# Kernel tuning notes

Hardware: AMD Instinct MI355X
Metric: run time of the kernel (lower is better)

## Reference

```python
import jax, jax.numpy as jnp
import numpy as np

B, M, H, D = 2, 16384, 8, 64
HID = H * D
SEG = 128          # segment_lengths[0]
DIL = 2            # dilation_rates[0]


def _hilbert_perm(m):
    """perm[d] = row-major token index of the d-th point on the Hilbert curve
    over an n x n grid (n = sqrt(m), power of 2). Vectorized d2xy."""
    n = int(round(np.sqrt(m)))
    assert n * n == m and (n & (n - 1)) == 0
    t = np.arange(m, dtype=np.int64)
    x = np.zeros(m, np.int64)
    y = np.zeros(m, np.int64)
    s = 1
    while s < n:
        rx = 1 & (t // 2)
        ry = 1 & (t ^ rx)
        swap = ry == 0
        flip = swap & (rx == 1)
        xf = np.where(flip, s - 1 - x, x)
        yf = np.where(flip, s - 1 - y, y)
        x, y = np.where(swap, yf, xf), np.where(swap, xf, yf)
        x = x + s * rx
        y = y + s * ry
        t = t // 4
        s *= 2
    return y * n + x


_PERM = _hilbert_perm(M)
_INV = np.empty(M, np.int64)
_INV[_PERM] = np.arange(M)
PERM = jnp.asarray(_PERM)
INV_PERM = jnp.asarray(_INV)


def setup_inputs() -> dict:
    key = jax.random.key(0)
    ks = jax.random.split(key, 8)
    sc = 0.02
    return {
        "q": jax.random.normal(ks[0], (B, M, H, D), jnp.float32),
        "k": jax.random.normal(ks[1], (B, M, H, D), jnp.float32),
        "v": jax.random.normal(ks[2], (B, M, H, D), jnp.float32),
        # wrapper projections (nn.Linear without bias; stored [in, out])
        "Wq": jax.random.normal(ks[3], (HID, HID), jnp.float32) * sc,
        "Wk": jax.random.normal(ks[4], (HID, HID), jnp.float32) * sc,
        "Wv": jax.random.normal(ks[5], (HID, HID), jnp.float32) * sc,
        # HilbertAttentionCore fused qkv projection
        "Wqkv": jax.random.normal(ks[6], (HID, 3 * HID), jnp.float32) * sc,
        # wrapper output projection
        "Wout": jax.random.normal(ks[7], (HID, HID), jnp.float32) * sc,
    }


def _hilbert_attention(x, Wqkv):
    """x: [B, M, HID] -> [B, M, HID]. Hilbert reorder + segmented dilated attn."""
    b, m, _ = x.shape
    qkv = x @ Wqkv                                    # [B, M, 3*HID]
    qkv = qkv.reshape(b, m, 3, H, D)
    # Hilbert-curve reordering of the sequence (gather)
    qkv = qkv[:, PERM]                                # [B, M, 3, H, D]
    nseg = m // SEG
    g = SEG // DIL                                    # tokens per dilated group
    # [B, nseg, g, DIL, 3, H, D]: group r holds positions r, r+DIL, ... in seg
    qkv = qkv.reshape(b, nseg, g, DIL, 3, H, D)
    qh, kh, vh = qkv[..., 0, :, :], qkv[..., 1, :, :], qkv[..., 2, :, :]
    scale = 1.0 / jnp.sqrt(jnp.asarray(D, x.dtype))
    # attention within each (segment, dilation-group): t,s index the g tokens
    scores = jnp.einsum("bntrhd,bnsrhd->bnrhts", qh, kh) * scale
    attn = jax.nn.softmax(scores, axis=-1)
    out = jnp.einsum("bnrhts,bnsrhd->bntrhd", attn, vh)
    out = out.reshape(b, m, H, D)
    # inverse Hilbert reordering (scatter back)
    out = out[:, INV_PERM]
    return out.reshape(b, m, HID)


def reference(q, k, v, Wq, Wk, Wv, Wqkv, Wout):
    b, m, h, d = q.shape
    q_flat = q.reshape(b, m, h * d)
    k_flat = k.reshape(b, m, h * d)
    v_flat = v.reshape(b, m, h * d)
    x = (q_flat @ Wq + k_flat @ Wk + v_flat @ Wv) / 3.0
    out = _hilbert_attention(x, Wqkv)
    out = out @ Wout
    return out.reshape(b, m, h, d)
```

## Files before the change

### kernel.cpp

```cpp
#include <hip/hip_runtime.h>
#include <hip/hip_bf16.h>
#include <stdint.h>


typedef __bf16 bf16_t;
typedef __bf16 bf16x8 __attribute__((ext_vector_type(8)));
typedef float  f32x4  __attribute__((ext_vector_type(4)));

#define DEVI __device__ __forceinline__
#define BAR __builtin_amdgcn_s_barrier()

static constexpr int Mtok = 16384;
static constexpr int ROWS = 32768;

DEVI void gload_lds16(const void* g, void* l) {
  __builtin_amdgcn_global_load_lds(
      (__attribute__((address_space(1))) uint32_t*)(uintptr_t)g,
      (__attribute__((address_space(3))) uint32_t*)(uint32_t)(uintptr_t)l,
      16, 0, 0);
}

DEVI void xcd_swizzle(int gx, int* bx, int* by) {
  int nwg = gx * gridDim.y;
  int wg = blockIdx.x + gx * blockIdx.y;
  int swz = (wg & 7) * (nwg >> 3) + (wg >> 3);
  *bx = swz % gx;
  *by = swz / gx;
}

__global__ void k_perm(int* __restrict__ perm) {
  int d = blockIdx.x * 256 + threadIdx.x;
  if (d >= Mtok) return;
  int t = d, x = 0, y = 0;
  for (int s = 1; s < 128; s <<= 1) {
    int rx = (t >> 1) & 1;
    int ry = (t ^ rx) & 1;
    if (ry == 0) {
      if (rx == 1) { x = s - 1 - x; y = s - 1 - y; }
      int tmp = x; x = y; y = tmp;
    }
    x += s * rx;
    y += s * ry;
    t >>= 2;
  }
  perm[d] = y * 128 + x;
}

__global__ void k_prep_w(const float* __restrict__ Wq, const float* __restrict__ Wk,
                         const float* __restrict__ Wv, const float* __restrict__ Wqkv,
                         const float* __restrict__ Wout,
                         bf16_t* __restrict__ W1t, bf16_t* __restrict__ Wqkvt,
                         bf16_t* __restrict__ Woutt) {
  const int tid = blockIdx.x * 256 + threadIdx.x;
  const int stride = gridDim.x * 256;
  for (int i = tid; i < 512 * 1536; i += stride) {
    int n = i / 1536, kk = i % 1536;
    const float* W = (kk < 512) ? Wq : (kk < 1024 ? Wk : Wv);
    W1t[i] = (bf16_t)(W[(kk & 511) * 512 + n] * (1.0f / 3.0f));
  }
  for (int i = tid; i < 1536 * 512; i += stride) {
    int n = i / 512, kk = i % 512;
    Wqkvt[i] = (bf16_t)Wqkv[kk * 1536 + n];
  }
  for (int i = tid; i < 512 * 512; i += stride) {
    int n = i / 512, kk = i % 512;
    Woutt[i] = (bf16_t)Wout[kk * 512 + n];
  }
}

DEVI void stageB(const bf16_t* Bb, int Kdim, int k0, bf16_t* dst, int qsel,
                 int tid, int cswz) {
  int r = tid >> 3;
  int rb0 = (r >> 5) * 64 + qsel * 32 + (r & 31);
  const bf16_t* g = Bb + (long)rb0 * Kdim + k0 + cswz * 8;
  gload_lds16(g, dst + rb0 * 64 + (tid & 7) * 8);
  gload_lds16(g + (long)128 * Kdim, dst + (rb0 + 128) * 64 + (tid & 7) * 8);
}

DEVI void stageA(const bf16_t* Ab, int Kdim, int k0, bf16_t* dst, int qsel,
                 int tid, int cswz) {
  int r = tid >> 3;
  int row0 = r + qsel * 64;
  const bf16_t* g = Ab + (long)row0 * Kdim + k0 + cswz * 8;
  gload_lds16(g, dst + row0 * 64 + (tid & 7) * 8);
  gload_lds16(g + (long)128 * Kdim, dst + (row0 + 128) * 64 + (tid & 7) * 8);
}

#define LOAD_AF(AF, QM, BUF)                                                   \
  _Pragma("unroll") for (int m = 0; m < 4; m++) {                              \
    int row = wm * 128 + (QM) * 64 + m * 16 + l15;                             \
    AF[m][0] = *(const bf16x8*)((BUF) + row * 64 + cb0 * 8);                   \
    AF[m][1] = *(const bf16x8*)((BUF) + row * 64 + cb1 * 8);                   \
  }
#define LOAD_BG(BG, QN, BUF)                                                   \
  _Pragma("unroll") for (int n = 0; n < 2; n++) {                              \
    int row = wn * 64 + (QN) * 32 + n * 16 + l15;                              \
    BG[n][0] = *(const bf16x8*)((BUF) + row * 64 + cb0 * 8);                   \
    BG[n][1] = *(const bf16x8*)((BUF) + row * 64 + cb1 * 8);                   \
  }
#define QUAD(QM, QN, AF, BG)                                                   \
  do {                                                                         \
    __builtin_amdgcn_s_setprio(1);                                             \
    _Pragma("unroll") for (int kh = 0; kh < 2; kh++)                           \
    _Pragma("unroll") for (int m = 0; m < 4; m++)                              \
    _Pragma("unroll") for (int n = 0; n < 2; n++)                              \
      acc[(QM)*4+m][(QN)*2+n] = __builtin_amdgcn_mfma_f32_16x16x32_bf16(       \
          AF[m][kh], BG[n][kh], acc[(QM)*4+m][(QN)*2+n], 0, 0, 0);             \
    __builtin_amdgcn_s_setprio(0);                                             \
  } while (0)

template <bool OUTF32>
__global__ __launch_bounds__(512, 2) void k_gemm256(const bf16_t* __restrict__ A,
                                                    const bf16_t* __restrict__ Bt,
                                                    bf16_t* __restrict__ Cb,
                                                    float* __restrict__ Cf,
                                                    int Ndim, int Kdim) {
  __shared__ bf16_t lds[4 * 16384];
  const int tid = threadIdx.x;
  const int lane = tid & 63, w = tid >> 6;
  const int wm = w >> 2, wn = w & 3;
  const int l15 = lane & 15, l4 = lane >> 4;
  const int cb0 = l4 ^ (l15 & 7), cb1 = cb0 ^ 4;
  const int cswz = (tid & 7) ^ ((tid >> 3) & 7);
  int bx, by;
  xcd_swizzle(gridDim.x, &bx, &by);
  const long arow0 = (long)by * 256;
  const long bcol0 = (long)bx * 256;
  const bf16_t* Ab = A + arow0 * Kdim;
  const bf16_t* Bb = Bt + bcol0 * Kdim;
  const int NT = Kdim >> 6;

  bf16_t* Acur = lds;
  bf16_t* Bcur = lds + 16384;
  bf16_t* Anxt = lds + 32768;
  bf16_t* Bnxt = lds + 49152;

  f32x4 acc[8][4] = {};

  stageA(Ab, Kdim, 0, Acur, 0, tid, cswz);
  stageA(Ab, Kdim, 0, Acur, 1, tid, cswz);
  stageB(Bb, Kdim, 0, Bcur, 0, tid, cswz);
  stageB(Bb, Kdim, 0, Bcur, 1, tid, cswz);
  stageA(Ab, Kdim, 64, Anxt, 0, tid, cswz);
  stageB(Bb, Kdim, 64, Bnxt, 1, tid, cswz);
  asm volatile("s_waitcnt vmcnt(4)" ::: "memory");
  BAR;

  for (int t = 0; t < NT; t++) {
    bf16x8 af[4][2], bg0[2][2], bg1[2][2];
    LOAD_AF(af, 0, Acur);
    LOAD_BG(bg0, 0, Bcur);
    if (t + 1 < NT) stageB(Bb, Kdim, (t + 1) * 64, Bnxt, 0, tid, cswz);
    QUAD(0, 0, af, bg0);
    BAR;
    LOAD_BG(bg1, 1, Bcur);
    if (t + 1 < NT) stageA(Ab, Kdim, (t + 1) * 64, Anxt, 1, tid, cswz);
    QUAD(0, 1, af, bg1);
    BAR;
    LOAD_AF(af, 1, Acur);
    if (t + 2 < NT) stageA(Ab, Kdim, (t + 2) * 64, Acur, 0, tid, cswz);
    QUAD(1, 1, af, bg1);
    BAR;
    LOAD_BG(bg0, 0, Bcur);
    if (t + 2 < NT) stageB(Bb, Kdim, (t + 2) * 64, Bcur, 1, tid, cswz);
    QUAD(1, 0, af, bg0);
    if (t + 2 < NT) { asm volatile("s_waitcnt vmcnt(4)" ::: "memory"); }
    else            { asm volatile("s_waitcnt vmcnt(0)" ::: "memory"); }
    BAR;
    bf16_t* tA = Acur; Acur = Anxt; Anxt = tA;
    bf16_t* tB = Bcur; Bcur = Bnxt; Bnxt = tB;
  }

#pragma unroll
  for (int i = 0; i < 8; i++) {
#pragma unroll
    for (int j = 0; j < 4; j++) {
      long row = arow0 + wm * 128 + i * 16 + l4 * 4;
      long col = bcol0 + wn * 64 + j * 16 + l15;
#pragma unroll
      for (int r = 0; r < 4; r++) {
        if constexpr (OUTF32) Cf[(row + r) * Ndim + col] = acc[i][j][r];
        else                  Cb[(row + r) * Ndim + col] = (bf16_t)acc[i][j][r];
      }
    }
  }
}

DEVI const float* selsrc(int tt, const float* q, const float* k, const float* v) {
  return tt < 8 ? q : (tt < 16 ? k : v);
}

DEVI void loadAh(const float* S, long grow, int colf, float4* pa) {
  const float* p0 = S + grow * 512 + colf;
  pa[0] = *(const float4*)(p0);
  pa[1] = *(const float4*)(p0 + 4);
  const float* p1 = p0 + 128 * 512;
  pa[2] = *(const float4*)(p1);
  pa[3] = *(const float4*)(p1 + 4);
}

DEVI void writeAh(bf16_t* dst, int rbase, int cbt, const float4* pa) {
  bf16x8 o0, o1;
  o0[0] = (bf16_t)pa[0].x; o0[1] = (bf16_t)pa[0].y; o0[2] = (bf16_t)pa[0].z; o0[3] = (bf16_t)pa[0].w;
  o0[4] = (bf16_t)pa[1].x; o0[5] = (bf16_t)pa[1].y; o0[6] = (bf16_t)pa[1].z; o0[7] = (bf16_t)pa[1].w;
  o1[0] = (bf16_t)pa[2].x; o1[1] = (bf16_t)pa[2].y; o1[2] = (bf16_t)pa[2].z; o1[3] = (bf16_t)pa[2].w;
  o1[4] = (bf16_t)pa[3].x; o1[5] = (bf16_t)pa[3].y; o1[6] = (bf16_t)pa[3].z; o1[7] = (bf16_t)pa[3].w;
  int sw = (cbt ^ (rbase & 7)) * 8;
  *(bf16x8*)(dst + rbase * 64 + sw) = o0;
  *(bf16x8*)(dst + (rbase + 128) * 64 + sw) = o1;
}

__global__ __launch_bounds__(512, 2) void k_gemm1f(const float* __restrict__ q,
                                                   const float* __restrict__ k,
                                                   const float* __restrict__ v,
                                                   const bf16_t* __restrict__ Bt,
                                                   bf16_t* __restrict__ Cb,
                                                   int Ndim) {
  constexpr int Kdim = 1536;
  constexpr int NT = 24;
  __shared__ bf16_t lds[4 * 16384];
  const int tid = threadIdx.x;
  const int lane = tid & 63, w = tid >> 6;
  const int wm = w >> 2, wn = w & 3;
  const int l15 = lane & 15, l4 = lane >> 4;
  const int cb0 = l4 ^ (l15 & 7), cb1 = cb0 ^ 4;
  const int cswz = (tid & 7) ^ ((tid >> 3) & 7);
  const int cbt = tid & 7, rA = tid >> 3;
  int bx, by;
  xcd_swizzle(gridDim.x, &bx, &by);
  const long arow0 = (long)by * 256;
  const long bcol0 = (long)bx * 256;
  const bf16_t* Bb = Bt + bcol0 * Kdim;

  bf16_t* Acur = lds;
  bf16_t* Bcur = lds + 16384;
  bf16_t* Anxt = lds + 32768;
  bf16_t* Bnxt = lds + 49152;

  f32x4 acc[8][4] = {};
  float4 pa0[4], pa1[4];

  loadAh(selsrc(0, q, k, v), arow0 + rA,      (cbt << 3), pa0);
  loadAh(selsrc(0, q, k, v), arow0 + rA + 64, (cbt << 3), pa1);
  writeAh(Acur, rA,      cbt, pa0);
  writeAh(Acur, rA + 64, cbt, pa1);
  stageB(Bb, Kdim, 0, Bcur, 0, tid, cswz);
  stageB(Bb, Kdim, 0, Bcur, 1, tid, cswz);
  loadAh(selsrc(1, q, k, v), arow0 + rA, 64 + (cbt << 3), pa0);
  writeAh(Anxt, rA, cbt, pa0);
  stageB(Bb, Kdim, 64, Bnxt, 1, tid, cswz);
  loadAh(selsrc(1, q, k, v), arow0 + rA + 64,  64 + (cbt << 3), pa1);
  loadAh(selsrc(2, q, k, v), arow0 + rA,      128 + (cbt << 3), pa0);
  asm volatile("s_waitcnt vmcnt(10)" ::: "memory");
  asm volatile("s_waitcnt lgkmcnt(0)" ::: "memory");
  BAR;

  for (int t = 0; t < NT; t++) {
    bf16x8 af[4][2], bg0[2][2], bg1[2][2];
    LOAD_AF(af, 0, Acur);
    LOAD_BG(bg0, 0, Bcur);
    if (t + 1 < NT) stageB(Bb, Kdim, (t + 1) * 64, Bnxt, 0, tid, cswz);
    QUAD(0, 0, af, bg0);
    BAR;
    LOAD_BG(bg1, 1, Bcur);
    if (t + 1 < NT) writeAh(Anxt, rA + 64, cbt, pa1);
    if (t + 2 < NT) loadAh(selsrc(t + 2, q, k, v), arow0 + rA + 64,
                           (((t + 2) & 7) << 6) + (cbt << 3), pa1);
    QUAD(0, 1, af, bg1);
    BAR;
    LOAD_AF(af, 1, Acur);
    if (t + 2 < NT) writeAh(Acur, rA, cbt, pa0);
    if (t + 3 < NT) loadAh(selsrc(t + 3, q, k, v), arow0 + rA,
                           (((t + 3) & 7) << 6) + (cbt << 3), pa0);
    QUAD(1, 1, af, bg1);
    BAR;
    LOAD_BG(bg0, 0, Bcur);
    if (t + 2 < NT) stageB(Bb, Kdim, (t + 2) * 64, Bcur, 1, tid, cswz);
    QUAD(1, 0, af, bg0);
    if (t + 3 < NT)      { asm volatile("s_waitcnt vmcnt(10)" ::: "memory"); }
    else if (t + 2 < NT) { asm volatile("s_waitcnt vmcnt(6)"  ::: "memory"); }
    else                 { asm volatile("s_waitcnt vmcnt(0)"  ::: "memory"); }
    asm volatile("s_waitcnt lgkmcnt(0)" ::: "memory");
    BAR;
    bf16_t* tA = Acur; Acur = Anxt; Anxt = tA;
    bf16_t* tB = Bcur; Bcur = Bnxt; Bnxt = tB;
  }

#pragma unroll
  for (int i = 0; i < 8; i++) {
#pragma unroll
    for (int j = 0; j < 4; j++) {
      long row = arow0 + wm * 128 + i * 16 + l4 * 4;
      long col = bcol0 + wn * 64 + j * 16 + l15;
#pragma unroll
      for (int r = 0; r < 4; r++)
        Cb[(row + r) * Ndim + col] = (bf16_t)acc[i][j][r];
    }
  }
}

__global__ __launch_bounds__(256, 2) void k_attn(const bf16_t* __restrict__ QKV,
                                                 const int* __restrict__ perm,
                                                 bf16_t* __restrict__ ATT) {
  __shared__ bf16_t Vt[2][64 * 64];
  __shared__ bf16_t P[2][64 * 64];
  __shared__ bf16_t O[128 * 64];
  __shared__ int perml[128];
  const int n = blockIdx.x, h = blockIdx.y, b = blockIdx.z;
  const int t = threadIdx.x;
  const int lane = t & 63, w = t >> 6;
  const int l15 = lane & 15, l4 = lane >> 4;

  if (t < 128) perml[t] = perm[n * 128 + t];
  __syncthreads();

#pragma unroll
  for (int it = 0; it < 4; it++) {
    int c = t + it * 256;
    int tok = c >> 3, c8 = c & 7;
    long j = (long)b * Mtok + perml[tok];
    bf16x8 vv = *(const bf16x8*)(QKV + j * 1536 + 1024 + h * 64 + c8 * 8);
    int grp = tok & 1, s = tok >> 1;
    bf16_t* vt = Vt[grp];
#pragma unroll
    for (int i = 0; i < 8; i++) {
      int d = c8 * 8 + i;
      vt[d * 64 + (s ^ ((d & 7) << 3))] = vv[i];
    }
  }

  const int grp = w >> 1, th = w & 1;

  f32x4 sc[2][4] = {};
#pragma unroll
  for (int ks = 0; ks < 2; ks++) {
    bf16x8 aq[2], bk[4];
#pragma unroll
    for (int tf = 0; tf < 2; tf++) {
      int tq = th * 32 + tf * 16 + l15;
      long j = (long)b * Mtok + perml[tq * 2 + grp];
      aq[tf] = *(const bf16x8*)(QKV + j * 1536 + h * 64 + ks * 32 + l4 * 8);
    }
#pragma unroll
    for (int sf = 0; sf < 4; sf++) {
      int s = sf * 16 + l15;
      long j = (long)b * Mtok + perml[s * 2 + grp];
      bk[sf] = *(const bf16x8*)(QKV + j * 1536 + 512 + h * 64 + ks * 32 + l4 * 8);
    }
#pragma unroll
    for (int tf = 0; tf < 2; tf++)
#pragma unroll
      for (int sf = 0; sf < 4; sf++)
        sc[tf][sf] = __builtin_amdgcn_mfma_f32_16x16x32_bf16(aq[tf], bk[sf], sc[tf][sf], 0, 0, 0);
  }

  const float scale = 0.125f;
#pragma unroll
  for (int tf = 0; tf < 2; tf++) {
#pragma unroll
    for (int r = 0; r < 4; r++) {
      float mx = fmaxf(fmaxf(sc[tf][0][r], sc[tf][1][r]), fmaxf(sc[tf][2][r], sc[tf][3][r]));
      mx = fmaxf(mx, __shfl_xor(mx, 1, 64));
      mx = fmaxf(mx, __shfl_xor(mx, 2, 64));
      mx = fmaxf(mx, __shfl_xor(mx, 4, 64));
      mx = fmaxf(mx, __shfl_xor(mx, 8, 64));
      float p0 = __expf((sc[tf][0][r] - mx) * scale);
      float p1 = __expf((sc[tf][1][r] - mx) * scale);
      float p2 = __expf((sc[tf][2][r] - mx) * scale);
      float p3 = __expf((sc[tf][3][r] - mx) * scale);
      float sum = p0 + p1 + p2 + p3;
      sum += __shfl_xor(sum, 1, 64);
      sum += __shfl_xor(sum, 2, 64);
      sum += __shfl_xor(sum, 4, 64);
      sum += __shfl_xor(sum, 8, 64);
      float inv = 1.0f / sum;
      int trow = th * 32 + tf * 16 + l4 * 4 + r;
      int sw = (trow & 7) << 3;
      bf16_t* pp = P[grp];
      pp[trow * 64 + ((l15     ) ^ sw)] = (bf16_t)(p0 * inv);
      pp[trow * 64 + ((l15 + 16) ^ sw)] = (bf16_t)(p1 * inv);
      pp[trow * 64 + ((l15 + 32) ^ sw)] = (bf16_t)(p2 * inv);
      pp[trow * 64 + ((l15 + 48) ^ sw)] = (bf16_t)(p3 * inv);
    }
  }
  __syncthreads();

  f32x4 oacc[2][4] = {};
#pragma unroll
  for (int ks = 0; ks < 2; ks++) {
    bf16x8 ap[2], bv[4];
#pragma unroll
    for (int tf = 0; tf < 2; tf++) {
      int trow = th * 32 + tf * 16 + l15;
      int cb = (ks * 4 + l4) ^ (trow & 7);
      ap[tf] = *(const bf16x8*)(P[grp] + trow * 64 + cb * 8);
    }
#pragma unroll
    for (int df = 0; df < 4; df++) {
      int d = df * 16 + l15;
      int cb = (ks * 4 + l4) ^ (d & 7);
      bv[df] = *(const bf16x8*)(Vt[grp] + d * 64 + cb * 8);
    }
#pragma unroll
    for (int tf = 0; tf < 2; tf++)
#pragma unroll
      for (int df = 0; df < 4; df++)
        oacc[tf][df] = __builtin_amdgcn_mfma_f32_16x16x32_bf16(ap[tf], bv[df], oacc[tf][df], 0, 0, 0);
  }

#pragma unroll
  for (int tf = 0; tf < 2; tf++)
#pragma unroll
    for (int df = 0; df < 4; df++)
#pragma unroll
      for (int r = 0; r < 4; r++) {
        int trow = th * 32 + tf * 16 + l4 * 4 + r;
        int tok = trow * 2 + grp;
        O[tok * 64 + df * 16 + l15] = (bf16_t)oacc[tf][df][r];
      }
  __syncthreads();
#pragma unroll
  for (int it = 0; it < 4; it++) {
    int c = t + it * 256;
    int tok = c >> 3, c8 = c & 7;
    long j = (long)b * Mtok + perml[tok];
    *(bf16x8*)(ATT + j * 512 + h * 64 + c8 * 8) = *(const bf16x8*)(O + tok * 64 + c8 * 8);
  }
}

extern "C" void kernel_launch(void* const* d_in, const int* in_sizes, int n_in,
                              void* d_out, int out_size, void* d_ws, size_t ws_size,
                              hipStream_t stream) {
  const float* q    = (const float*)d_in[0];
  const float* k    = (const float*)d_in[1];
  const float* v    = (const float*)d_in[2];
  const float* Wq   = (const float*)d_in[3];
  const float* Wk   = (const float*)d_in[4];
  const float* Wv   = (const float*)d_in[5];
  const float* Wqkv = (const float*)d_in[6];
  const float* Wout = (const float*)d_in[7];

  char* ws = (char*)d_ws;
  const size_t QKV_BYTES = (size_t)ROWS * 1536 * 2;
  const size_t X_BYTES   = (size_t)ROWS * 512 * 2;
  bf16_t* QKV   = (bf16_t*)ws;
  bf16_t* X     = (bf16_t*)(ws + QKV_BYTES);
  bf16_t* W1t   = (bf16_t*)(ws + QKV_BYTES + X_BYTES);
  bf16_t* Wqkvt = W1t + 512 * 1536;
  bf16_t* Woutt = Wqkvt + 1536 * 512;
  int*    perm  = (int*)(Woutt + 512 * 512);

  k_perm<<<64, 256, 0, stream>>>(perm);
  k_prep_w<<<512, 256, 0, stream>>>(Wq, Wk, Wv, Wqkv, Wout, W1t, Wqkvt, Woutt);
  k_gemm1f<<<dim3(2, 128), 512, 0, stream>>>(q, k, v, W1t, X, 512);
  k_gemm256<false><<<dim3(6, 128), 512, 0, stream>>>(X, Wqkvt, QKV, nullptr, 1536, 512);
  k_attn<<<dim3(128, 8, 2), 256, 0, stream>>>(QKV, perm, X);
  k_gemm256<true><<<dim3(2, 128), 512, 0, stream>>>(X, Woutt, nullptr, (float*)d_out, 512, 512);
}
```

Before: 210.6 us.

## Replace 256x256 GEMM with 128x128 tile kernel for QKV and output projections

```diff
diff --git a/kernel.cpp b/kernel.cpp
--- a/kernel.cpp
+++ b/kernel.cpp
@@ -9,6 +9,7 @@
 
 #define DEVI __device__ __forceinline__
 #define BAR __builtin_amdgcn_s_barrier()
+#define CFENCE asm volatile("" ::: "memory")
 
 static constexpr int Mtok = 16384;
 static constexpr int ROWS = 32768;
@@ -22,6 +23,7 @@
 
 DEVI void xcd_swizzle(int gx, int* bx, int* by) {
   int nwg = gx * gridDim.y;
+  if (nwg & 7) { *bx = blockIdx.x; *by = blockIdx.y; return; }
   int wg = blockIdx.x + gx * blockIdx.y;
   int swz = (wg & 7) * (nwg >> 3) + (wg >> 3);
   *bx = swz % gx;
@@ -77,15 +79,6 @@
   gload_lds16(g + (long)128 * Kdim, dst + (rb0 + 128) * 64 + (tid & 7) * 8);
 }
 
-DEVI void stageA(const bf16_t* Ab, int Kdim, int k0, bf16_t* dst, int qsel,
-                 int tid, int cswz) {
-  int r = tid >> 3;
-  int row0 = r + qsel * 64;
-  const bf16_t* g = Ab + (long)row0 * Kdim + k0 + cswz * 8;
-  gload_lds16(g, dst + row0 * 64 + (tid & 7) * 8);
-  gload_lds16(g + (long)128 * Kdim, dst + (row0 + 128) * 64 + (tid & 7) * 8);
-}
-
 #define LOAD_AF(AF, QM, BUF)                                                   \
   _Pragma("unroll") for (int m = 0; m < 4; m++) {                              \
     int row = wm * 128 + (QM) * 64 + m * 16 + l15;                             \
@@ -108,83 +101,6 @@
           AF[m][kh], BG[n][kh], acc[(QM)*4+m][(QN)*2+n], 0, 0, 0);             \
     __builtin_amdgcn_s_setprio(0);                                             \
   } while (0)
-
-template <bool OUTF32>
-__global__ __launch_bounds__(512, 2) void k_gemm256(const bf16_t* __restrict__ A,
-                                                    const bf16_t* __restrict__ Bt,
-                                                    bf16_t* __restrict__ Cb,
-                                                    float* __restrict__ Cf,
-                                                    int Ndim, int Kdim) {
-  __shared__ bf16_t lds[4 * 16384];
-  const int tid = threadIdx.x;
-  const int lane = tid & 63, w = tid >> 6;
-  const int wm = w >> 2, wn = w & 3;
-  const int l15 = lane & 15, l4 = lane >> 4;
-  const int cb0 = l4 ^ (l15 & 7), cb1 = cb0 ^ 4;
-  const int cswz = (tid & 7) ^ ((tid >> 3) & 7);
-  int bx, by;
-  xcd_swizzle(gridDim.x, &bx, &by);
-  const long arow0 = (long)by * 256;
-  const long bcol0 = (long)bx * 256;
-  const bf16_t* Ab = A + arow0 * Kdim;
-  const bf16_t* Bb = Bt + bcol0 * Kdim;
-  const int NT = Kdim >> 6;
-
-  bf16_t* Acur = lds;
-  bf16_t* Bcur = lds + 16384;
-  bf16_t* Anxt = lds + 32768;
-  bf16_t* Bnxt = lds + 49152;
-
-  f32x4 acc[8][4] = {};
-
-  stageA(Ab, Kdim, 0, Acur, 0, tid, cswz);
-  stageA(Ab, Kdim, 0, Acur, 1, tid, cswz);
-  stageB(Bb, Kdim, 0, Bcur, 0, tid, cswz);
-  stageB(Bb, Kdim, 0, Bcur, 1, tid, cswz);
-  stageA(Ab, Kdim, 64, Anxt, 0, tid, cswz);
-  stageB(Bb, Kdim, 64, Bnxt, 1, tid, cswz);
-  asm volatile("s_waitcnt vmcnt(4)" ::: "memory");
-  BAR;
-
-  for (int t = 0; t < NT; t++) {
-    bf16x8 af[4][2], bg0[2][2], bg1[2][2];
-    LOAD_AF(af, 0, Acur);
-    LOAD_BG(bg0, 0, Bcur);
-    if (t + 1 < NT) stageB(Bb, Kdim, (t + 1) * 64, Bnxt, 0, tid, cswz);
-    QUAD(0, 0, af, bg0);
-    BAR;
-    LOAD_BG(bg1, 1, Bcur);
-    if (t + 1 < NT) stageA(Ab, Kdim, (t + 1) * 64, Anxt, 1, tid, cswz);
-    QUAD(0, 1, af, bg1);
-    BAR;
-    LOAD_AF(af, 1, Acur);
-    if (t + 2 < NT) stageA(Ab, Kdim, (t + 2) * 64, Acur, 0, tid, cswz);
-    QUAD(1, 1, af, bg1);
-    BAR;
-    LOAD_BG(bg0, 0, Bcur);
-    if (t + 2 < NT) stageB(Bb, Kdim, (t + 2) * 64, Bcur, 1, tid, cswz);
-    QUAD(1, 0, af, bg0);
-    if (t + 2 < NT) { asm volatile("s_waitcnt vmcnt(4)" ::: "memory"); }
-    else            { asm volatile("s_waitcnt vmcnt(0)" ::: "memory"); }
-    BAR;
-    bf16_t* tA = Acur; Acur = Anxt; Anxt = tA;
-    bf16_t* tB = Bcur; Bcur = Bnxt; Bnxt = tB;
-  }
-
-#pragma unroll
-  for (int i = 0; i < 8; i++) {
-#pragma unroll
-    for (int j = 0; j < 4; j++) {
-      long row = arow0 + wm * 128 + i * 16 + l4 * 4;
-      long col = bcol0 + wn * 64 + j * 16 + l15;
-#pragma unroll
-      for (int r = 0; r < 4; r++) {
-        if constexpr (OUTF32) Cf[(row + r) * Ndim + col] = acc[i][j][r];
-        else                  Cb[(row + r) * Ndim + col] = (bf16_t)acc[i][j][r];
-      }
-    }
-  }
-}
 
 DEVI const float* selsrc(int tt, const float* q, const float* k, const float* v) {
   return tt < 8 ? q : (tt < 16 ? k : v);
@@ -295,6 +211,113 @@
 #pragma unroll
       for (int r = 0; r < 4; r++)
         Cb[(row + r) * Ndim + col] = (bf16_t)acc[i][j][r];
+    }
+  }
+}
+
+#define FRAGS_128                                                              \
+  bf16x8 af[4][2], bg[4][2];                                                   \
+  _Pragma("unroll") for (int m = 0; m < 4; m++) {                              \
+    int row = wm * 64 + m * 16 + l15;                                          \
+    af[m][0] = *(const bf16x8*)(Al + row * 64 + cb0 * 8);                      \
+    af[m][1] = *(const bf16x8*)(Al + row * 64 + cb1 * 8);                      \
+  }                                                                            \
+  _Pragma("unroll") for (int n = 0; n < 4; n++) {                              \
+    int row = wn * 64 + n * 16 + l15;                                          \
+    bg[n][0] = *(const bf16x8*)(Bl + row * 64 + cb0 * 8);                      \
+    bg[n][1] = *(const bf16x8*)(Bl + row * 64 + cb1 * 8);                      \
+  }
+
+#define MFMA_128                                                               \
+  __builtin_amdgcn_s_setprio(1);                                               \
+  _Pragma("unroll") for (int kh = 0; kh < 2; kh++)                             \
+  _Pragma("unroll") for (int m = 0; m < 4; m++)                                \
+  _Pragma("unroll") for (int n = 0; n < 4; n++)                                \
+    acc[m][n] = __builtin_amdgcn_mfma_f32_16x16x32_bf16(af[m][kh], bg[n][kh],  \
+                                                        acc[m][n], 0, 0, 0);   \
+  __builtin_amdgcn_s_setprio(0);
+
+template <bool OUTF32, int KD>
+__global__ __launch_bounds__(256, 2) void k_gemm128(const bf16_t* __restrict__ A,
+                                                    const bf16_t* __restrict__ Bt,
+                                                    bf16_t* __restrict__ Cb,
+                                                    float* __restrict__ Cf,
+                                                    int Ndim) {
+  constexpr int NT = KD / 64;
+  __shared__ bf16_t lds[4][8192];
+  const int tid = threadIdx.x, lane = tid & 63, w = tid >> 6;
+  const int wm = w >> 1, wn = w & 1;
+  const int l15 = lane & 15, l4 = lane >> 4;
+  const int cb0 = l4 ^ (l15 & 7), cb1 = cb0 ^ 4;
+  int bx, by;
+  xcd_swizzle(gridDim.x, &bx, &by);
+  const long arow0 = (long)by * 128;
+  const long bcol0 = (long)bx * 128;
+
+  auto stage = [&](int t, int buf) {
+#pragma unroll
+    for (int j = 0; j < 4; j++) {
+      int cc = tid + j * 256;
+      int row = cc >> 3;
+      int sw = ((cc & 7) ^ (row & 7)) * 8;
+      gload_lds16(A + (arow0 + row) * KD + t * 64 + sw, &lds[buf * 2][cc * 8]);
+      gload_lds16(Bt + (bcol0 + row) * KD + t * 64 + sw, &lds[buf * 2 + 1][cc * 8]);
+    }
+  };
+
+  f32x4 acc[4][4] = {};
+
+  stage(0, 0);
+  CFENCE;
+  stage(1, 1);
+  CFENCE;
+  asm volatile("s_waitcnt vmcnt(8)" ::: "memory");
+  BAR;
+  CFENCE;
+
+  for (int t = 0; t < NT - 2; t++) {
+    const bf16_t* Al = lds[(t & 1) * 2];
+    const bf16_t* Bl = lds[(t & 1) * 2 + 1];
+    FRAGS_128;
+    asm volatile("s_waitcnt lgkmcnt(0)" ::: "memory");
+    BAR;
+    CFENCE;
+    stage(t + 2, t & 1);
+    CFENCE;
+    MFMA_128;
+    asm volatile("s_waitcnt vmcnt(8)" ::: "memory");
+    BAR;
+    CFENCE;
+  }
+  {
+    const bf16_t* Al = lds[(NT & 1) * 2];
+    const bf16_t* Bl = lds[(NT & 1) * 2 + 1];
+    FRAGS_128;
+    asm volatile("s_waitcnt lgkmcnt(0)" ::: "memory");
+    BAR;
+    MFMA_128;
+    asm volatile("s_waitcnt vmcnt(0)" ::: "memory");
+    BAR;
+    CFENCE;
+  }
+  {
+    const bf16_t* Al = lds[((NT - 1) & 1) * 2];
+    const bf16_t* Bl = lds[((NT - 1) & 1) * 2 + 1];
+    FRAGS_128;
+    MFMA_128;
+  }
+
+#pragma unroll
+  for (int m = 0; m < 4; m++) {
+#pragma unroll
+    for (int n = 0; n < 4; n++) {
+      long row = arow0 + wm * 64 + m * 16 + l4 * 4;
+      long col = bcol0 + wn * 64 + n * 16 + l15;
+#pragma unroll
+      for (int r = 0; r < 4; r++) {
+        if constexpr (OUTF32) Cf[(row + r) * Ndim + col] = acc[m][n][r];
+        else                  Cb[(row + r) * Ndim + col] = (bf16_t)acc[m][n][r];
+      }
     }
   }
 }
@@ -453,7 +476,7 @@
   k_perm<<<64, 256, 0, stream>>>(perm);
   k_prep_w<<<512, 256, 0, stream>>>(Wq, Wk, Wv, Wqkv, Wout, W1t, Wqkvt, Woutt);
   k_gemm1f<<<dim3(2, 128), 512, 0, stream>>>(q, k, v, W1t, X, 512);
-  k_gemm256<false><<<dim3(6, 128), 512, 0, stream>>>(X, Wqkvt, QKV, nullptr, 1536, 512);
+  k_gemm128<false, 512><<<dim3(12, 256), 256, 0, stream>>>(X, Wqkvt, QKV, nullptr, 1536);
   k_attn<<<dim3(128, 8, 2), 256, 0, stream>>>(QKV, perm, X);
-  k_gemm256<true><<<dim3(2, 128), 512, 0, stream>>>(X, Woutt, nullptr, (float*)d_out, 512, 512);
-}
+  k_gemm128<true, 512><<<dim3(4, 256), 256, 0, stream>>>(X, Woutt, nullptr, (float*)d_out, 512);
+}
```

Result: faster. 203.2 us (-3.5%).
